# Performance work log

Hardware: AMD Instinct MI355X
Metric: run time of the kernel (lower is better)

## Reference

```python
import jax, jax.numpy as jnp
import numpy as np

B, H, W, C, NH, WS, SS = 32, 56, 56, 192, 6, 7, 3
N = WS * WS
HD = C // NH
NW = (H // WS) * (W // WS)
HID = 4 * C
RPB_SIZE = (2 * WS - 1) * (2 * WS - 1)


def _rel_index():
    coords = np.stack(np.meshgrid(np.arange(WS), np.arange(WS), indexing='ij')).reshape(2, -1)
    rel = (coords[:, :, None] - coords[:, None, :]).transpose(1, 2, 0)
    rel[..., 0] += WS - 1
    rel[..., 1] += WS - 1
    rel[..., 0] *= 2 * WS - 1
    return rel.sum(-1)  # (N, N) int

REL_IDX = jnp.asarray(_rel_index())


def _swin_attn_mask():
    # standard Swin shifted-window mask: -100 for cross-region pairs
    img = np.zeros((H, W))
    cnt = 0
    for hs in (slice(0, -WS), slice(-WS, -SS), slice(-SS, None)):
        for ws_ in (slice(0, -WS), slice(-WS, -SS), slice(-SS, None)):
            img[hs, ws_] = cnt
            cnt += 1
    win = img.reshape(H // WS, WS, W // WS, WS).transpose(0, 2, 1, 3).reshape(-1, N)
    diff = win[:, None, :] - win[:, :, None]
    return np.where(diff != 0, -100.0, 0.0).astype(np.float32)  # (NW, N, N)


def _ln(t, g, b, eps=1e-5):
    mu = t.mean(-1, keepdims=True)
    v = ((t - mu) ** 2).mean(-1, keepdims=True)
    return (t - mu) * jax.lax.rsqrt(v + eps) * g + b


def setup_inputs() -> dict:
    key = jax.random.key(0)
    ks = jax.random.split(key, 12)
    s = 0.02
    return {
        'x': jax.random.normal(ks[0], (B, H * W, C), jnp.float32),
        'attn_mask': jnp.asarray(_swin_attn_mask()),
        'ln1_g': jnp.ones((C,), jnp.float32),
        'ln1_b': jnp.zeros((C,), jnp.float32),
        'qkv_w': jax.random.normal(ks[1], (C, 3 * C), jnp.float32) * s,
        'qkv_b': jnp.zeros((3 * C,), jnp.float32),
        'rpb': jax.random.normal(ks[2], (RPB_SIZE, NH), jnp.float32) * s,
        'proj_w': jax.random.normal(ks[3], (C, C), jnp.float32) * s,
        'proj_b': jnp.zeros((C,), jnp.float32),
        'ln2_g': jnp.ones((C,), jnp.float32),
        'ln2_b': jnp.zeros((C,), jnp.float32),
        'fc1_w': jax.random.normal(ks[4], (C, HID), jnp.float32) * s,
        'fc1_b': jnp.zeros((HID,), jnp.float32),
        'fc2_w': jax.random.normal(ks[5], (HID, C), jnp.float32) * s,
        'fc2_b': jnp.zeros((C,), jnp.float32),
    }


def reference(x, attn_mask, ln1_g, ln1_b, qkv_w, qkv_b, rpb, proj_w, proj_b,
              ln2_g, ln2_b, fc1_w, fc1_b, fc2_w, fc2_b):
    shortcut = x
    h = _ln(x, ln1_g, ln1_b).reshape(B, H, W, C)
    # cyclic shift
    h = jnp.roll(h, (-SS, -SS), axis=(1, 2))
    # window partition -> (B*NW, N, C)
    h = h.reshape(B, H // WS, WS, W // WS, WS, C).transpose(0, 1, 3, 2, 4, 5).reshape(B * NW, N, C)
    qkv = (h @ qkv_w + qkv_b).reshape(B * NW, N, 3, NH, HD).transpose(2, 0, 3, 1, 4)
    q, k, v = qkv[0] * (HD ** -0.5), qkv[1], qkv[2]
    attn = jnp.einsum('bhnd,bhmd->bhnm', q, k)  # (B*NW, NH, N, N)
    bias = rpb[REL_IDX].transpose(2, 0, 1)      # (NH, N, N)
    attn = attn + bias[None]
    attn = attn.reshape(B, NW, NH, N, N) + attn_mask[None, :, None]
    attn = jax.nn.softmax(attn.reshape(B * NW, NH, N, N), axis=-1)
    o = jnp.einsum('bhnm,bhmd->bhnd', attn, v).transpose(0, 2, 1, 3).reshape(B * NW, N, C)
    o = o @ proj_w + proj_b
    # window reverse + reverse shift
    o = o.reshape(B, H // WS, W // WS, WS, WS, C).transpose(0, 1, 3, 2, 4, 5).reshape(B, H, W, C)
    o = jnp.roll(o, (SS, SS), axis=(1, 2)).reshape(B, H * W, C)
    x1 = shortcut + o
    m = _ln(x1, ln2_g, ln2_b)
    m = jax.nn.gelu(m @ fc1_w + fc1_b, approximate=False) @ fc2_w + fc2_b
    return x1 + m
```

## Files before the change

kernel.cpp:

```cpp
#include <hip/hip_runtime.h>
#include <hip/hip_bf16.h>

typedef __hip_bfloat16 bf16;
typedef __attribute__((ext_vector_type(8))) short short8;
typedef __attribute__((ext_vector_type(4))) float f32x4;
typedef __attribute__((ext_vector_type(4))) unsigned short ushort4_t;

#define TOK 100352
#define NWIN 2048
#define CC 192
#define NHEAD 6
#define NT 49

__device__ __forceinline__ float bf2f(bf16 v) { return __bfloat162float(v); }
__device__ __forceinline__ bf16 f2bf(float v) { return __float2bfloat16(v); }
__device__ __forceinline__ float b2f_bits(unsigned short u) {
    return __uint_as_float(((unsigned)u) << 16);
}

__device__ __forceinline__ float ldin(const void* p, size_t i, int f) {
    return f ? ((const float*)p)[i] : bf2f(((const bf16*)p)[i]);
}
__device__ __forceinline__ void stc(bf16* p, float v) { *p = f2bf(v); }
__device__ __forceinline__ void stc(float* p, float v) { *p = v; }
__device__ __forceinline__ float ldc(const bf16* p) { return bf2f(*p); }
__device__ __forceinline__ float ldc(const float* p) { return *p; }

__device__ __forceinline__ float gelu_f(float v) {
    float z = v * 0.70710678118654752f;
    float az = fabsf(z);
    float t = __builtin_amdgcn_rcpf(1.0f + 0.3275911f * az);
    float p = t * (0.254829592f + t * (-0.284496736f + t * (1.421413741f
            + t * (-1.453152027f + t * 1.061405429f))));
    float e = __expf(-az * az);
    float er = copysignf(1.0f - p * e, z);
    return 0.5f * v * (1.0f + er);
}

__device__ __forceinline__ void gl_lds16(const bf16* g, bf16* l) {
    __builtin_amdgcn_global_load_lds(
        (const __attribute__((address_space(1))) unsigned int*)g,
        (__attribute__((address_space(3))) unsigned int*)l, 16, 0, 0);
}

__global__ void dtype_probe_kernel(const void* xraw, int* flag) {
    const unsigned short* u = (const unsigned short*)xraw;
    int lane = threadIdx.x & 63;
    int weird = 0;
    for (int i = lane; i < 4096; i += 64) {
        unsigned int bits = ((unsigned int)u[2 * i]) << 16;
        float v = __uint_as_float(bits);
        if (!(fabsf(v) <= 1e10f)) weird++;
    }
    #pragma unroll
    for (int off = 32; off > 0; off >>= 1) weird += __shfl_xor(weird, off, 64);
    if (lane == 0) *flag = (weird > 256) ? 1 : 0;
}

__global__ void transpose_kernel(const void* __restrict__ in, bf16* __restrict__ out,
                                 int K, int N, const int* __restrict__ flag) {
    int f = *flag;
    int idx = blockIdx.x * 256 + threadIdx.x;
    if (idx >= K * N) return;
    int nn = idx / K, kk = idx % K;
    out[idx] = f2bf(ldin(in, (size_t)kk * N + nn, f));
}

__global__ __launch_bounds__(256) void comb_kernel(
    const void* __restrict__ rpb, const void* __restrict__ mask,
    bf16* __restrict__ comb, const int* __restrict__ flag) {
    int f = *flag;
    int idx = blockIdx.x * 256 + threadIdx.x;
    int m = idx & 63;
    int n = (idx >> 6) & 63;
    int hw = idx >> 12;
    int head = hw % NHEAD, wi = hw / NHEAD;
    float v;
    if (n < NT && m < NT) {
        int nr = n / 7, nc = n % 7, mr = m / 7, mc = m % 7;
        int ridx = (nr - mr + 6) * 13 + (nc - mc + 6);
        v = ldin(rpb, (size_t)ridx * NHEAD + head, f)
          + ldin(mask, (size_t)wi * NT * NT + n * NT + m, f);
    } else {
        v = -1e30f;
    }
    comb[idx] = f2bf(v);
}

__global__ __launch_bounds__(256) void ln1_window_kernel(
    const void* __restrict__ x, const void* __restrict__ g, const void* __restrict__ b,
    bf16* __restrict__ hwin, const int* __restrict__ flag) {
    int f = *flag;
    int wave = threadIdx.x >> 6, lane = threadIdx.x & 63;
    int t = blockIdx.x * 4 + wave;
    int bidx = t / (64 * NT);
    int r = t % (64 * NT);
    int wi = r / NT, n = r % NT;
    int wr = wi >> 3, wc = wi & 7;
    int nr = n / 7, nc = n % 7;
    int si = wr * 7 + nr, sj = wc * 7 + nc;
    int oi = si + 3; if (oi >= 56) oi -= 56;
    int oj = sj + 3; if (oj >= 56) oj -= 56;
    size_t src = ((size_t)bidx * 3136 + oi * 56 + oj) * CC;
    float v0 = ldin(x, src + lane, f);
    float v1 = ldin(x, src + lane + 64, f);
    float v2 = ldin(x, src + lane + 128, f);
    float s = v0 + v1 + v2;
    float sq = v0 * v0 + v1 * v1 + v2 * v2;
    #pragma unroll
    for (int off = 32; off > 0; off >>= 1) {
        s  += __shfl_xor(s, off, 64);
        sq += __shfl_xor(sq, off, 64);
    }
    float mu = s * (1.f / 192.f);
    float var = fmaxf(sq * (1.f / 192.f) - mu * mu, 0.f);
    float rs = rsqrtf(var + 1e-5f);
    bf16* dst = hwin + (size_t)t * CC;
    dst[lane]       = f2bf((v0 - mu) * rs * ldin(g, lane, f)       + ldin(b, lane, f));
    dst[lane + 64]  = f2bf((v1 - mu) * rs * ldin(g, lane + 64, f)  + ldin(b, lane + 64, f));
    dst[lane + 128] = f2bf((v2 - mu) * rs * ldin(g, lane + 128, f) + ldin(b, lane + 128, f));
}

template <int EPI, typename CT>
__global__ __launch_bounds__(256, 4) void gemm_kernel(
    const bf16* __restrict__ A, const bf16* __restrict__ Wt,
    const void* __restrict__ bias, CT* __restrict__ C,
    const CT* __restrict__ resid, int M, int K, int Nc, const int* __restrict__ flag) {
    int f = *flag;
    __shared__ __align__(16) bf16 sb[3][6144];
    int tid = threadIdx.x;
    int wave = tid >> 6, lane = tid & 63;
    int quad = lane >> 4, l16 = lane & 15;

    int nwg = gridDim.x * gridDim.y;
    int bid = blockIdx.y * gridDim.x + blockIdx.x;
    int swz = bid;
    if ((nwg & 7) == 0) {
        int cpx = nwg >> 3;
        swz = (bid & 7) * cpx + (bid >> 3);
    }
    int bn = swz % gridDim.x, bm = swz / gridDim.x;

    int swzk = (((lane & 3) ^ ((lane >> 3) & 3)) * 8);
    int q2   = (quad ^ ((l16 >> 1) & 3)) * 8;

    const bf16* ag[2];
    #pragma unroll
    for (int j = 0; j < 2; j++)
        ag[j] = A + (size_t)(bm * 128 + (wave * 2 + j) * 16 + (lane >> 2)) * K + swzk;
    const bf16* bg = Wt + (size_t)(bn * 64 + wave * 16 + (lane >> 2)) * K + swzk;

    auto STAGE = [&](int t, int buf) {
        gl_lds16(ag[0] + (size_t)t * 32, &sb[buf][(wave * 2 + 0) * 512]);
        gl_lds16(ag[1] + (size_t)t * 32, &sb[buf][(wave * 2 + 1) * 512]);
        gl_lds16(bg    + (size_t)t * 32, &sb[buf][4096 + wave * 512]);
    };

    f32x4 acc[2][4];
    #pragma unroll
    for (int i = 0; i < 2; i++)
        #pragma unroll
        for (int j = 0; j < 4; j++)
            acc[i][j][0] = acc[i][j][1] = acc[i][j][2] = acc[i][j][3] = 0.f;

    const int nt = K >> 5;

    STAGE(0, 0);
    STAGE(1, 1);
    asm volatile("s_waitcnt vmcnt(3)" ::: "memory");
    __builtin_amdgcn_s_barrier();

    int cur = 0;
    for (int t = 0; t < nt; t++) {
        if (t + 2 < nt) {
            int stg = cur + 2; if (stg >= 3) stg -= 3;
            STAGE(t + 2, stg);
        }
        const bf16* sA = &sb[cur][0];
        const bf16* sB = &sb[cur][4096];
        short8 av[2], bv[4];
        #pragma unroll
        for (int tm = 0; tm < 2; tm++)
            av[tm] = *(const short8*)(&sA[(wave * 32 + tm * 16 + l16) * 32 + q2]);
        #pragma unroll
        for (int tn = 0; tn < 4; tn++)
            bv[tn] = *(const short8*)(&sB[(tn * 16 + l16) * 32 + q2]);
        #pragma unroll
        for (int tm = 0; tm < 2; tm++)
            #pragma unroll
            for (int tn = 0; tn < 4; tn++)
                acc[tm][tn] = __builtin_amdgcn_mfma_f32_16x16x32_bf16(av[tm], bv[tn], acc[tm][tn], 0, 0, 0);
        if (t + 1 < nt) {
            if (t + 2 < nt)
                asm volatile("s_waitcnt vmcnt(3) lgkmcnt(0)" ::: "memory");
            else
                asm volatile("s_waitcnt vmcnt(0) lgkmcnt(0)" ::: "memory");
            __builtin_amdgcn_s_barrier();
        }
        cur++; if (cur >= 3) cur -= 3;
    }

    #pragma unroll
    for (int tm = 0; tm < 2; tm++)
        #pragma unroll
        for (int tn = 0; tn < 4; tn++) {
            int col = bn * 64 + tn * 16 + l16;
            float bvs = ldin(bias, col, f);
            #pragma unroll
            for (int r = 0; r < 4; r++) {
                int row = bm * 128 + wave * 32 + tm * 16 + quad * 4 + r;
                float v = acc[tm][tn][r] + bvs;
                if (EPI == 1) v = gelu_f(v);
                if (EPI == 2) v += ldc(&resid[(size_t)row * Nc + col]);
                stc(&C[(size_t)row * Nc + col], v);
            }
        }
}

__global__ __launch_bounds__(256) void attn_mfma_kernel(
    const bf16* __restrict__ qkv, const bf16* __restrict__ comb,
    bf16* __restrict__ attn_out, int wbase) {
    __shared__ __align__(16) bf16 Qs[64 * 40];
    __shared__ __align__(16) bf16 Ks[64 * 40];
    __shared__ __align__(16) bf16 Vt[32 * 72];
    __shared__ __align__(16) bf16 P[64 * 72];

    int head = blockIdx.x % NHEAD;
    int wl = blockIdx.x / NHEAD;
    int wg = wbase + wl;
    int wi = wg & 63;
    int t0 = wl * NT;
    int tg = wg * NT;
    int tid = threadIdx.x;
    int wave = tid >> 6, lane = tid & 63;
    int quad = lane >> 4, l16 = lane & 15;

    {
        int row = tid >> 2;
        int dc = (tid & 3) * 8;
        uint4 qv = make_uint4(0, 0, 0, 0), kv = qv, vv = qv;
        if (row < NT) {
            const bf16* base = qkv + (size_t)(t0 + row) * 576 + head * 32 + dc;
            qv = *(const uint4*)(base);
            kv = *(const uint4*)(base + 192);
            vv = *(const uint4*)(base + 384);
        }
        *(uint4*)(&Qs[row * 40 + dc]) = qv;
        *(uint4*)(&Ks[row * 40 + dc]) = kv;
        bf16 tv[8];
        *(uint4*)tv = vv;
        #pragma unroll
        for (int r = 0; r < 8; r++)
            Vt[(dc + r) * 72 + row] = tv[r];
    }
    __syncthreads();

    const float scale = 0.17677669529663687f;
    int tm = wave;
    int q = tm * 16 + l16;
    const bf16* crow = comb + (((size_t)wi * NHEAD + head) * 64 + q) * 64;

    ushort4_t cb[4];
    #pragma unroll
    for (int tn = 0; tn < 4; tn++)
        cb[tn] = *(const ushort4_t*)(crow + tn * 16 + quad * 4);

    float s[4][4];
    short8 bfrag = *(const short8*)(&Qs[q * 40 + quad * 8]);
    f32x4 z; z[0] = z[1] = z[2] = z[3] = 0.f;
    #pragma unroll
    for (int tn = 0; tn < 4; tn++) {
        short8 afrag = *(const short8*)(&Ks[(tn * 16 + l16) * 40 + quad * 8]);
        f32x4 acc = __builtin_amdgcn_mfma_f32_16x16x32_bf16(afrag, bfrag, z, 0, 0, 0);
        s[tn][0] = acc[0] * scale + b2f_bits(cb[tn][0]);
        s[tn][1] = acc[1] * scale + b2f_bits(cb[tn][1]);
        s[tn][2] = acc[2] * scale + b2f_bits(cb[tn][2]);
        s[tn][3] = acc[3] * scale + b2f_bits(cb[tn][3]);
    }

    float mx = s[0][0];
    #pragma unroll
    for (int tn = 0; tn < 4; tn++)
        #pragma unroll
        for (int r = 0; r < 4; r++) mx = fmaxf(mx, s[tn][r]);
    mx = fmaxf(mx, __shfl_xor(mx, 16, 64));
    mx = fmaxf(mx, __shfl_xor(mx, 32, 64));
    float sm = 0.f;
    #pragma unroll
    for (int tn = 0; tn < 4; tn++)
        #pragma unroll
        for (int r = 0; r < 4; r++) { s[tn][r] = __expf(s[tn][r] - mx); sm += s[tn][r]; }
    sm += __shfl_xor(sm, 16, 64);
    sm += __shfl_xor(sm, 32, 64);
    float inv = 1.0f / sm;

    #pragma unroll
    for (int tn = 0; tn < 4; tn++) {
        bf16 pk[4];
        #pragma unroll
        for (int r = 0; r < 4; r++) pk[r] = f2bf(s[tn][r] * inv);
        *(uint2*)(&P[q * 72 + tn * 16 + quad * 4]) = *(const uint2*)pk;
    }

    f32x4 oacc[2];
    oacc[0][0] = oacc[0][1] = oacc[0][2] = oacc[0][3] = 0.f;
    oacc[1] = oacc[0];
    #pragma unroll
    for (int kc = 0; kc < 2; kc++) {
        short8 pa = *(const short8*)(&P[(tm * 16 + l16) * 72 + kc * 32 + quad * 8]);
        #pragma unroll
        for (int tn = 0; tn < 2; tn++) {
            short8 vb = *(const short8*)(&Vt[(tn * 16 + l16) * 72 + kc * 32 + quad * 8]);
            oacc[tn] = __builtin_amdgcn_mfma_f32_16x16x32_bf16(pa, vb, oacc[tn], 0, 0, 0);
        }
    }
    #pragma unroll
    for (int tn = 0; tn < 2; tn++) {
        #pragma unroll
        for (int r = 0; r < 4; r++) {
            int n = tm * 16 + quad * 4 + r;
            int d = tn * 16 + l16;
            if (n < NT)
                attn_out[(size_t)(tg + n) * CC + head * 32 + d] = f2bf(oacc[tn][r]);
        }
    }
}

__global__ __launch_bounds__(256) void resid_ln2_kernel(
    const void* __restrict__ x, const bf16* __restrict__ proj,
    const void* __restrict__ g, const void* __restrict__ b,
    float* __restrict__ x1, bf16* __restrict__ h2, const int* __restrict__ flag) {
    int f = *flag;
    int wave = threadIdx.x >> 6, lane = threadIdx.x & 63;
    int tok = blockIdx.x * 4 + wave;
    int bidx = tok / 3136;
    int r = tok % 3136;
    int i = r / 56, j = r % 56;
    int si = i + 53; if (si >= 56) si -= 56;
    int sj = j + 53; if (sj >= 56) sj -= 56;
    int wi = (si / 7) * 8 + sj / 7;
    int n = (si % 7) * 7 + (sj % 7);
    size_t tw = ((size_t)bidx * 64 + wi) * NT + n;
    const bf16* ps = proj + tw * CC;
    size_t xs = (size_t)tok * CC;
    float v0 = ldin(x, xs + lane, f)       + bf2f(ps[lane]);
    float v1 = ldin(x, xs + lane + 64, f)  + bf2f(ps[lane + 64]);
    float v2 = ldin(x, xs + lane + 128, f) + bf2f(ps[lane + 128]);
    float* xd = x1 + (size_t)tok * CC;
    xd[lane] = v0; xd[lane + 64] = v1; xd[lane + 128] = v2;
    float s = v0 + v1 + v2;
    float sq = v0 * v0 + v1 * v1 + v2 * v2;
    #pragma unroll
    for (int off = 32; off > 0; off >>= 1) {
        s  += __shfl_xor(s, off, 64);
        sq += __shfl_xor(sq, off, 64);
    }
    float mu = s * (1.f / 192.f);
    float var = fmaxf(sq * (1.f / 192.f) - mu * mu, 0.f);
    float rs = rsqrtf(var + 1e-5f);
    bf16* dst = h2 + (size_t)tok * CC;
    dst[lane]       = f2bf((v0 - mu) * rs * ldin(g, lane, f)       + ldin(b, lane, f));
    dst[lane + 64]  = f2bf((v1 - mu) * rs * ldin(g, lane + 64, f)  + ldin(b, lane + 64, f));
    dst[lane + 128] = f2bf((v2 - mu) * rs * ldin(g, lane + 128, f) + ldin(b, lane + 128, f));
}

extern "C" void kernel_launch(void* const* d_in, const int* in_sizes, int n_in,
                              void* d_out, int out_size, void* d_ws, size_t ws_size,
                              hipStream_t stream) {
    const void* x        = d_in[0];
    const void* attnmask = d_in[1];
    const void* ln1_g    = d_in[2];
    const void* ln1_b    = d_in[3];
    const void* qkv_w    = d_in[4];
    const void* qkv_b    = d_in[5];
    const void* rpb      = d_in[6];
    const void* proj_w   = d_in[7];
    const void* proj_b   = d_in[8];
    const void* ln2_g    = d_in[9];
    const void* ln2_b    = d_in[10];
    const void* fc1_w    = d_in[11];
    const void* fc1_b    = d_in[12];
    const void* fc2_w    = d_in[13];
    const void* fc2_b    = d_in[14];
    float* out = (float*)d_out;
    char* ws = (char*)d_ws;

    const size_t RSZ = (size_t)TOK * CC * sizeof(bf16);
    const size_t WEXT = 442368 * sizeof(bf16)
                      + (size_t)64 * NHEAD * 64 * 64 * sizeof(bf16)
                      + 64;
    const size_t NEED_BIG = 5 * RSZ + WEXT;

    const int M = TOK;

    if (ws_size >= NEED_BIG) {
        bf16* h_win    = (bf16*)(ws);
        bf16* qkvbuf   = (bf16*)(ws + RSZ);
        bf16* attn_out = (bf16*)(ws + 4 * RSZ);
        bf16* projbuf  = (bf16*)(ws);
        bf16* h2       = (bf16*)(ws + 4 * RSZ);
        bf16* m1buf    = (bf16*)(ws);
        bf16* qkvT     = (bf16*)(ws + 5 * RSZ);
        bf16* projT    = qkvT + 192 * 576;
        bf16* fc1T     = projT + 192 * 192;
        bf16* fc2T     = fc1T + 192 * 768;
        bf16* combT    = fc2T + 768 * 192;
        int*  flag     = (int*)(combT + 64 * NHEAD * 64 * 64);

        dtype_probe_kernel<<<1, 64, 0, stream>>>(x, flag);
        transpose_kernel<<<(192 * 576 + 255) / 256, 256, 0, stream>>>(qkv_w, qkvT, 192, 576, flag);
        transpose_kernel<<<(192 * 192 + 255) / 256, 256, 0, stream>>>(proj_w, projT, 192, 192, flag);
        transpose_kernel<<<(192 * 768 + 255) / 256, 256, 0, stream>>>(fc1_w, fc1T, 192, 768, flag);
        transpose_kernel<<<(768 * 192 + 255) / 256, 256, 0, stream>>>(fc2_w, fc2T, 768, 192, flag);
        comb_kernel<<<(64 * NHEAD * 64 * 64) / 256, 256, 0, stream>>>(rpb, attnmask, combT, flag);

        ln1_window_kernel<<<TOK / 4, 256, 0, stream>>>(x, ln1_g, ln1_b, h_win, flag);

        gemm_kernel<0, bf16><<<dim3(576 / 64, M / 128), 256, 0, stream>>>(
            h_win, qkvT, qkv_b, qkvbuf, (const bf16*)nullptr, M, 192, 576, flag);
        attn_mfma_kernel<<<NWIN * NHEAD, 256, 0, stream>>>(qkvbuf, combT, attn_out, 0);

        gemm_kernel<0, bf16><<<dim3(192 / 64, M / 128), 256, 0, stream>>>(
            attn_out, projT, proj_b, projbuf, (const bf16*)nullptr, M, 192, 192, flag);

        resid_ln2_kernel<<<TOK / 4, 256, 0, stream>>>(x, projbuf, ln2_g, ln2_b, out, h2, flag);

        gemm_kernel<1, bf16><<<dim3(768 / 64, M / 128), 256, 0, stream>>>(
            h2, fc1T, fc1_b, m1buf, (const bf16*)nullptr, M, 192, 768, flag);
        gemm_kernel<2, float><<<dim3(192 / 64, M / 128), 256, 0, stream>>>(
            m1buf, fc2T, fc2_b, out, (const float*)out, M, 768, 192, flag);
    } else {
        bf16* h_win    = (bf16*)(ws);
        bf16* m1buf    = (bf16*)(ws);
        bf16* attn_out = (bf16*)(ws + RSZ);
        bf16* h2       = (bf16*)(ws + RSZ);
        bf16* qkvchunk = (bf16*)(ws + 2 * RSZ);
        bf16* projbuf  = (bf16*)(ws + 2 * RSZ);
        bf16* combT    = (bf16*)(ws + 2 * RSZ + 28901376);
        bf16* qkvT     = (bf16*)(ws + 3 * RSZ);
        bf16* projT    = qkvT + 192 * 576;
        bf16* fc1T     = projT + 192 * 192;
        bf16* fc2T     = fc1T + 192 * 768;
        int*  flag     = (int*)(fc2T + 768 * 192);

        dtype_probe_kernel<<<1, 64, 0, stream>>>(x, flag);
        transpose_kernel<<<(192 * 576 + 255) / 256, 256, 0, stream>>>(qkv_w, qkvT, 192, 576, flag);
        transpose_kernel<<<(192 * 192 + 255) / 256, 256, 0, stream>>>(proj_w, projT, 192, 192, flag);
        transpose_kernel<<<(192 * 768 + 255) / 256, 256, 0, stream>>>(fc1_w, fc1T, 192, 768, flag);
        transpose_kernel<<<(768 * 192 + 255) / 256, 256, 0, stream>>>(fc2_w, fc2T, 768, 192, flag);
        comb_kernel<<<(64 * NHEAD * 64 * 64) / 256, 256, 0, stream>>>(rpb, attnmask, combT, flag);

        ln1_window_kernel<<<TOK / 4, 256, 0, stream>>>(x, ln1_g, ln1_b, h_win, flag);

        const int QCH = 4, QW = NWIN / QCH;
        const int QROWS = QW * NT;
        for (int c = 0; c < QCH; c++) {
            const bf16* a = h_win + (size_t)c * QROWS * CC;
            gemm_kernel<0, bf16><<<dim3(576 / 64, QROWS / 128), 256, 0, stream>>>(
                a, qkvT, qkv_b, qkvchunk, (const bf16*)nullptr, QROWS, 192, 576, flag);
            attn_mfma_kernel<<<QW * NHEAD, 256, 0, stream>>>(
                qkvchunk, combT, attn_out, c * QW);
        }

        gemm_kernel<0, bf16><<<dim3(192 / 64, M / 128), 256, 0, stream>>>(
            attn_out, projT, proj_b, projbuf, (const bf16*)nullptr, M, 192, 192, flag);

        resid_ln2_kernel<<<TOK / 4, 256, 0, stream>>>(x, projbuf, ln2_g, ln2_b, out, h2, flag);

        const int MCH = 4, MR = TOK / MCH;
        for (int c = 0; c < MCH; c++) {
            const bf16* a = h2 + (size_t)c * MR * CC;
            float* oc = out + (size_t)c * MR * CC;
            gemm_kernel<1, bf16><<<dim3(768 / 64, MR / 128), 256, 0, stream>>>(
                a, fc1T, fc1_b, m1buf, (const bf16*)nullptr, MR, 192, 768, flag);
            gemm_kernel<2, float><<<dim3(192 / 64, MR / 128), 256, 0, stream>>>(
                m1buf, fc2T, fc2_b, oc, (const float*)oc, MR, 768, 192, flag);
        }
    }
}
```

Measured before the change: 527.7 us.

## Fuse weight-prep launches and chunk the MLP GEMMs into two halves

The four weight-transpose kernels and the bias/mask combine kernel become a single prep_kernel launch, which removes four launches of small work. In the big-workspace path the fc1/fc2 MLP pair now runs in two row chunks, so the m1 intermediate written by fc1 is half the size and is more likely to stay in cache before fc2 reads it back. The cost is extra launches in the MLP and smaller grids per GEMM.

Result: faster. 508.8 us (-3.6%).

```diff
diff --git a/kernel.cpp b/kernel.cpp
--- a/kernel.cpp
+++ b/kernel.cpp
@@ -57,34 +57,56 @@
     if (lane == 0) *flag = (weird > 256) ? 1 : 0;
 }
 
-__global__ void transpose_kernel(const void* __restrict__ in, bf16* __restrict__ out,
-                                 int K, int N, const int* __restrict__ flag) {
-    int f = *flag;
-    int idx = blockIdx.x * 256 + threadIdx.x;
-    if (idx >= K * N) return;
-    int nn = idx / K, kk = idx % K;
-    out[idx] = f2bf(ldin(in, (size_t)kk * N + nn, f));
-}
-
-__global__ __launch_bounds__(256) void comb_kernel(
+__global__ __launch_bounds__(256) void prep_kernel(
+    const void* __restrict__ qkv_w, const void* __restrict__ proj_w,
+    const void* __restrict__ fc1_w, const void* __restrict__ fc2_w,
     const void* __restrict__ rpb, const void* __restrict__ mask,
+    bf16* __restrict__ qkvT, bf16* __restrict__ projT,
+    bf16* __restrict__ fc1T, bf16* __restrict__ fc2T,
     bf16* __restrict__ comb, const int* __restrict__ flag) {
     int f = *flag;
     int idx = blockIdx.x * 256 + threadIdx.x;
-    int m = idx & 63;
-    int n = (idx >> 6) & 63;
-    int hw = idx >> 12;
-    int head = hw % NHEAD, wi = hw / NHEAD;
-    float v;
-    if (n < NT && m < NT) {
-        int nr = n / 7, nc = n % 7, mr = m / 7, mc = m % 7;
-        int ridx = (nr - mr + 6) * 13 + (nc - mc + 6);
-        v = ldin(rpb, (size_t)ridx * NHEAD + head, f)
-          + ldin(mask, (size_t)wi * NT * NT + n * NT + m, f);
-    } else {
-        v = -1e30f;
-    }
-    comb[idx] = f2bf(v);
+    const int S1 = 192 * 576, S2 = 192 * 192, S3 = 192 * 768, S4 = 768 * 192;
+    if (idx < S1) {
+        int nn = idx / 192, kk = idx % 192;
+        qkvT[idx] = f2bf(ldin(qkv_w, (size_t)kk * 576 + nn, f));
+        return;
+    }
+    idx -= S1;
+    if (idx < S2) {
+        int nn = idx / 192, kk = idx % 192;
+        projT[idx] = f2bf(ldin(proj_w, (size_t)kk * 192 + nn, f));
+        return;
+    }
+    idx -= S2;
+    if (idx < S3) {
+        int nn = idx / 192, kk = idx % 192;
+        fc1T[idx] = f2bf(ldin(fc1_w, (size_t)kk * 768 + nn, f));
+        return;
+    }
+    idx -= S3;
+    if (idx < S4) {
+        int nn = idx / 768, kk = idx % 768;
+        fc2T[idx] = f2bf(ldin(fc2_w, (size_t)kk * 192 + nn, f));
+        return;
+    }
+    idx -= S4;
+    {
+        int m = idx & 63;
+        int n = (idx >> 6) & 63;
+        int hw = idx >> 12;
+        int head = hw % NHEAD, wi = hw / NHEAD;
+        float v;
+        if (n < NT && m < NT) {
+            int nr = n / 7, nc = n % 7, mr = m / 7, mc = m % 7;
+            int ridx = (nr - mr + 6) * 13 + (nc - mc + 6);
+            v = ldin(rpb, (size_t)ridx * NHEAD + head, f)
+              + ldin(mask, (size_t)wi * NT * NT + n * NT + m, f);
+        } else {
+            v = -1e30f;
+        }
+        comb[idx] = f2bf(v);
+    }
 }
 
 __global__ __launch_bounds__(256) void ln1_window_kernel(
@@ -392,6 +414,8 @@
     const size_t NEED_BIG = 5 * RSZ + WEXT;
 
     const int M = TOK;
+    const int PREP_ELEMS = 192 * 576 + 192 * 192 + 192 * 768 + 768 * 192
+                         + 64 * NHEAD * 64 * 64;
 
     if (ws_size >= NEED_BIG) {
         bf16* h_win    = (bf16*)(ws);
@@ -408,11 +432,9 @@
         int*  flag     = (int*)(combT + 64 * NHEAD * 64 * 64);
 
         dtype_probe_kernel<<<1, 64, 0, stream>>>(x, flag);
-        transpose_kernel<<<(192 * 576 + 255) / 256, 256, 0, stream>>>(qkv_w, qkvT, 192, 576, flag);
-        transpose_kernel<<<(192 * 192 + 255) / 256, 256, 0, stream>>>(proj_w, projT, 192, 192, flag);
-        transpose_kernel<<<(192 * 768 + 255) / 256, 256, 0, stream>>>(fc1_w, fc1T, 192, 768, flag);
-        transpose_kernel<<<(768 * 192 + 255) / 256, 256, 0, stream>>>(fc2_w, fc2T, 768, 192, flag);
-        comb_kernel<<<(64 * NHEAD * 64 * 64) / 256, 256, 0, stream>>>(rpb, attnmask, combT, flag);
+        prep_kernel<<<PREP_ELEMS / 256, 256, 0, stream>>>(
+            qkv_w, proj_w, fc1_w, fc2_w, rpb, attnmask,
+            qkvT, projT, fc1T, fc2T, combT, flag);
 
         ln1_window_kernel<<<TOK / 4, 256, 0, stream>>>(x, ln1_g, ln1_b, h_win, flag);
 
@@ -425,10 +447,15 @@
 
         resid_ln2_kernel<<<TOK / 4, 256, 0, stream>>>(x, projbuf, ln2_g, ln2_b, out, h2, flag);
 
-        gemm_kernel<1, bf16><<<dim3(768 / 64, M / 128), 256, 0, stream>>>(
-            h2, fc1T, fc1_b, m1buf, (const bf16*)nullptr, M, 192, 768, flag);
-        gemm_kernel<2, float><<<dim3(192 / 64, M / 128), 256, 0, stream>>>(
-            m1buf, fc2T, fc2_b, out, (const float*)out, M, 768, 192, flag);
+        const int MCH = 2, MR = TOK / MCH;
+        for (int c = 0; c < MCH; c++) {
+            const bf16* a = h2 + (size_t)c * MR * CC;
+            float* oc = out + (size_t)c * MR * CC;
+            gemm_kernel<1, bf16><<<dim3(768 / 64, MR / 128), 256, 0, stream>>>(
+                a, fc1T, fc1_b, m1buf, (const bf16*)nullptr, MR, 192, 768, flag);
+            gemm_kernel<2, float><<<dim3(192 / 64, MR / 128), 256, 0, stream>>>(
+                m1buf, fc2T, fc2_b, oc, (const float*)oc, MR, 768, 192, flag);
+        }
     } else {
         bf16* h_win    = (bf16*)(ws);
         bf16* m1buf    = (bf16*)(ws);
@@ -444,11 +471,9 @@
         int*  flag     = (int*)(fc2T + 768 * 192);
 
         dtype_probe_kernel<<<1, 64, 0, stream>>>(x, flag);
-        transpose_kernel<<<(192 * 576 + 255) / 256, 256, 0, stream>>>(qkv_w, qkvT, 192, 576, flag);
-        transpose_kernel<<<(192 * 192 + 255) / 256, 256, 0, stream>>>(proj_w, projT, 192, 192, flag);
-        transpose_kernel<<<(192 * 768 + 255) / 256, 256, 0, stream>>>(fc1_w, fc1T, 192, 768, flag);
-        transpose_kernel<<<(768 * 192 + 255) / 256, 256, 0, stream>>>(fc2_w, fc2T, 768, 192, flag);
-        comb_kernel<<<(64 * NHEAD * 64 * 64) / 256, 256, 0, stream>>>(rpb, attnmask, combT, flag);
+        prep_kernel<<<PREP_ELEMS / 256, 256, 0, stream>>>(
+            qkv_w, proj_w, fc1_w, fc2_w, rpb, attnmask,
+            qkvT, projT, fc1T, fc2T, combT, flag);
 
         ln1_window_kernel<<<TOK / 4, 256, 0, stream>>>(x, ln1_g, ln1_b, h_win, flag);
 
```
